# Performance work log

Hardware: AMD Instinct MI355X
Metric: run time of the kernel (lower is better)

## Reference

```python
import jax, jax.numpy as jnp
import numpy as np

ALPHA = 0.2  # LeakyReLU negative slope
NEG_BIG = -9e15


def setup_inputs() -> dict:
    key = jax.random.key(0)
    k1, k2, k3, k4 = jax.random.split(key, 4)
    N, F_IN, F_OUT = 8192, 256, 64
    h = jax.random.normal(k1, (N, F_IN), dtype=jnp.float32)
    # binary dense adjacency (density ~0.5), kept as float32 as in the torch code
    adj = jax.random.randint(k2, (N, N), 0, 2).astype(jnp.float32)
    W = jax.random.normal(k3, (F_IN, F_OUT), dtype=jnp.float32) * 0.05
    a = jax.random.normal(k4, (2 * F_OUT, 1), dtype=jnp.float32) * 0.05
    return {"h": h, "adj": adj, "W": W, "a": a}


def reference(h, adj, W, a):
    F_OUT = W.shape[1]
    Wh = h @ W                               # [N, F]
    # Decomposed concat-attention score: e_ij = LeakyReLU(a1.Wh_i + a2.Wh_j)
    f_src = Wh @ a[:F_OUT, 0]                # [N]
    f_dst = Wh @ a[F_OUT:, 0]                # [N]
    e = f_src[:, None] + f_dst[None, :]      # [N, N]
    e = jnp.where(e > 0, e, ALPHA * e)       # LeakyReLU
    e = jnp.where(adj > 0, e, NEG_BIG)       # mask non-edges
    attention = jax.nn.softmax(e, axis=1)    # row softmax (dropout p=0 -> identity)
    h_prime = attention @ (adj @ Wh)         # note: double propagation as in source
    # concat=True -> ELU
    return jnp.where(h_prime > 0, h_prime, jnp.expm1(h_prime))
```

## Files before the change

### kernel.cpp

```cpp
#include <hip/hip_runtime.h>
#include <hip/hip_bf16.h>


#define N 8192

typedef float f32x4 __attribute__((ext_vector_type(4)));
typedef short s16x8 __attribute__((ext_vector_type(8)));
typedef unsigned long long u64;
typedef u64 u64x2 __attribute__((ext_vector_type(2)));

__device__ __forceinline__ unsigned short f2bf(float x) {
  unsigned u = __float_as_uint(x);
  u += 0x7FFFu + ((u >> 16) & 1u);
  return (unsigned short)(u >> 16);
}
__device__ __forceinline__ unsigned pack2(unsigned short lo, unsigned short hi) {
  return (unsigned)lo | ((unsigned)hi << 16);
}

#define MFMA __builtin_amdgcn_mfma_f32_16x16x32_bf16

__global__ __launch_bounds__(256) void kA(const float* __restrict__ adj,
                                          const float* __restrict__ h,
                                          const float* __restrict__ W,
                                          const float* __restrict__ a,
                                          u64* __restrict__ ML,
                                          unsigned short* __restrict__ Bpack,
                                          float* __restrict__ f,
                                          float* __restrict__ g) {
  const int l = threadIdx.x & 63;
  const int w = threadIdx.x >> 6;
  const int bid = blockIdx.x;
  if ((bid & 1) == 0) {
    const int i = ((bid >> 1) << 2) + w;
    const float* ap = adj + (size_t)i * N + (l << 2);
    u64* mp = ML + (size_t)i * 128;
    f32x4 v0 = *(const f32x4*)(ap);
    f32x4 v1 = *(const f32x4*)(ap + 256);
    f32x4 v2 = *(const f32x4*)(ap + 512);
    f32x4 v3 = *(const f32x4*)(ap + 768);
    for (int cc = 0; cc < 32; cc += 4) {
      const int cn = (cc < 28) ? (cc + 4) : cc;
      f32x4 n0 = *(const f32x4*)(ap + ((cn + 0) << 8));
      f32x4 n1 = *(const f32x4*)(ap + ((cn + 1) << 8));
      f32x4 n2 = *(const f32x4*)(ap + ((cn + 2) << 8));
      f32x4 n3 = *(const f32x4*)(ap + ((cn + 3) << 8));
      u64 b0  = __ballot(v0.x > 0.f), b1  = __ballot(v0.y > 0.f);
      u64 b2  = __ballot(v0.z > 0.f), b3  = __ballot(v0.w > 0.f);
      u64 b4  = __ballot(v1.x > 0.f), b5  = __ballot(v1.y > 0.f);
      u64 b6  = __ballot(v1.z > 0.f), b7  = __ballot(v1.w > 0.f);
      u64 b8  = __ballot(v2.x > 0.f), b9  = __ballot(v2.y > 0.f);
      u64 b10 = __ballot(v2.z > 0.f), b11 = __ballot(v2.w > 0.f);
      u64 b12 = __ballot(v3.x > 0.f), b13 = __ballot(v3.y > 0.f);
      u64 b14 = __ballot(v3.z > 0.f), b15 = __ballot(v3.w > 0.f);
      if (l == 0) {
        u64x2* q = (u64x2*)(mp + (cc << 2));
        u64x2 t0; t0.x = b0;  t0.y = b1;  q[0] = t0;
        u64x2 t1; t1.x = b2;  t1.y = b3;  q[1] = t1;
        u64x2 t2; t2.x = b4;  t2.y = b5;  q[2] = t2;
        u64x2 t3; t3.x = b6;  t3.y = b7;  q[3] = t3;
        u64x2 t4; t4.x = b8;  t4.y = b9;  q[4] = t4;
        u64x2 t5; t5.x = b10; t5.y = b11; q[5] = t5;
        u64x2 t6; t6.x = b12; t6.y = b13; q[6] = t6;
        u64x2 t7; t7.x = b14; t7.y = b15; q[7] = t7;
      }
      v0 = n0; v1 = n1; v2 = n2; v3 = n3;
    }
  } else {
    const int i = ((bid >> 1) << 2) + w;
    const float* hrow = h + (size_t)i * 256;
    float acc = 0.f;
#pragma unroll 4
    for (int kb = 0; kb < 64; ++kb) {
      f32x4 hv = *(const f32x4*)(hrow + (kb << 2));
      acc += hv.x * W[((kb << 2) + 0) * 64 + l];
      acc += hv.y * W[((kb << 2) + 1) * 64 + l];
      acc += hv.z * W[((kb << 2) + 2) * 64 + l];
      acc += hv.w * W[((kb << 2) + 3) * 64 + l];
    }
    float s1 = acc * a[l];
    float s2 = acc * a[64 + l];
#pragma unroll
    for (int d = 32; d > 0; d >>= 1) {
      s1 += __shfl_xor(s1, d);
      s2 += __shfl_xor(s2, d);
    }
    if (l == 0) { f[i] = s1; g[i] = s2; }
    const int kb = i >> 5;
    const int b = l >> 4;
    const int lp = (l & 15) | (((i >> 3) & 3) << 4);
    const int e = i & 7;
    Bpack[(((size_t)(kb * 4 + b)) * 64 + lp) * 8 + e] = f2bf(acc);
  }
}

__global__ __launch_bounds__(512, 4) void k2b(const u64* __restrict__ ML,
                                              const unsigned short* __restrict__ Bpack,
                                              const float* __restrict__ g,
                                              unsigned short* __restrict__ Upack,
                                              float* __restrict__ Gmax) {
  __shared__ float red[8][64][16];
  __shared__ float gred[8][16];
  const int l = threadIdx.x & 63;
  const int w = threadIdx.x >> 6;
  const int i0 = blockIdx.x << 4;
  const int r = l & 15, kg = l >> 4;
  const s16x8* Bv = (const s16x8*)Bpack;
  const u64x2* mrow = (const u64x2*)(ML + (size_t)(i0 + r) * 128);
  const int sh0 = kg << 1;
  f32x4 acc0 = {0.f,0.f,0.f,0.f}, acc1 = acc0, acc2 = acc0, acc3 = acc0;
  float gmx = -INFINITY;
  for (int cc = 0; cc < 4; ++cc) {
    const int c = (w << 2) + cc;
    u64x2 m01 = mrow[(c << 1)], m23 = mrow[(c << 1) + 1];
    const u64 wq0 = m01.x >> sh0, wq1 = m01.y >> sh0,
              wq2 = m23.x >> sh0, wq3 = m23.y >> sh0;
#pragma unroll
    for (int j7 = 0; j7 < 8; ++j7) {
      const int jb = (c << 3) + j7;
      f32x4 g0 = *(const f32x4*)(g + (jb << 5) + (kg << 3));
      f32x4 g1 = *(const f32x4*)(g + (jb << 5) + (kg << 3) + 4);
      const unsigned bit0 = (unsigned)(wq0 >> (j7 << 3)) & 1u;
      const unsigned bit1 = (unsigned)(wq1 >> (j7 << 3)) & 1u;
      const unsigned bit2 = (unsigned)(wq2 >> (j7 << 3)) & 1u;
      const unsigned bit3 = (unsigned)(wq3 >> (j7 << 3)) & 1u;
      const unsigned bit4 = (unsigned)(wq0 >> ((j7 << 3) + 1)) & 1u;
      const unsigned bit5 = (unsigned)(wq1 >> ((j7 << 3) + 1)) & 1u;
      const unsigned bit6 = (unsigned)(wq2 >> ((j7 << 3) + 1)) & 1u;
      const unsigned bit7 = (unsigned)(wq3 >> ((j7 << 3) + 1)) & 1u;
      s16x8 af;
      af[0] = bit0 ? (short)0x3F80 : (short)0;
      af[1] = bit1 ? (short)0x3F80 : (short)0;
      af[2] = bit2 ? (short)0x3F80 : (short)0;
      af[3] = bit3 ? (short)0x3F80 : (short)0;
      af[4] = bit4 ? (short)0x3F80 : (short)0;
      af[5] = bit5 ? (short)0x3F80 : (short)0;
      af[6] = bit6 ? (short)0x3F80 : (short)0;
      af[7] = bit7 ? (short)0x3F80 : (short)0;
      if (bit0) gmx = fmaxf(gmx, g0.x);
      if (bit1) gmx = fmaxf(gmx, g0.y);
      if (bit2) gmx = fmaxf(gmx, g0.z);
      if (bit3) gmx = fmaxf(gmx, g0.w);
      if (bit4) gmx = fmaxf(gmx, g1.x);
      if (bit5) gmx = fmaxf(gmx, g1.y);
      if (bit6) gmx = fmaxf(gmx, g1.z);
      if (bit7) gmx = fmaxf(gmx, g1.w);
      const size_t bi = ((size_t)jb << 8) + l;
      s16x8 f0 = Bv[bi], f1 = Bv[bi + 64], f2 = Bv[bi + 128], f3 = Bv[bi + 192];
      acc0 = MFMA(af, f0, acc0, 0, 0, 0);
      acc1 = MFMA(af, f1, acc1, 0, 0, 0);
      acc2 = MFMA(af, f2, acc2, 0, 0, 0);
      acc3 = MFMA(af, f3, acc3, 0, 0, 0);
    }
  }
  gmx = fmaxf(gmx, __shfl_xor(gmx, 16));
  gmx = fmaxf(gmx, __shfl_xor(gmx, 32));
  if (l < 16) gred[w][l] = gmx;
#pragma unroll
  for (int q = 0; q < 4; ++q) {
    red[w][l][q] = acc0[q]; red[w][l][4 + q] = acc1[q];
    red[w][l][8 + q] = acc2[q]; red[w][l][12 + q] = acc3[q];
  }
  __syncthreads();
  const int tl = threadIdx.x & 63;
  const int b = (threadIdx.x >> 6) & 3;
  const int sE = threadIdx.x >> 8;
  const int reg0 = sE << 1;
  float u0 = 0.f, u1 = 0.f;
#pragma unroll
  for (int w8 = 0; w8 < 8; ++w8) {
    u0 += red[w8][tl][(b << 2) + reg0];
    u1 += red[w8][tl][(b << 2) + reg0 + 1];
  }
  const int k0 = i0 + ((tl >> 4) << 2) + reg0;
  const unsigned pkv = pack2(f2bf(u0), f2bf(u1));
  const int kbD = k0 >> 5, lgrp = (k0 >> 3) & 3, e0 = k0 & 7;
  *(unsigned*)((char*)Upack +
      ((size_t)((kbD << 2) + b) * 64 + ((tl & 15) | (lgrp << 4))) * 16 + (e0 << 1)) = pkv;
  if (threadIdx.x < 16) {
    float gm = gred[0][threadIdx.x];
#pragma unroll
    for (int w8 = 1; w8 < 8; ++w8) gm = fmaxf(gm, gred[w8][threadIdx.x]);
    Gmax[i0 + threadIdx.x] = gm;
  }
}

__global__ __launch_bounds__(512, 4) void k3(const u64* __restrict__ ML,
                                             const unsigned short* __restrict__ Upack,
                                             const float* __restrict__ f,
                                             const float* __restrict__ g,
                                             const float* __restrict__ Gmax,
                                             float* __restrict__ out) {
  __shared__ float red[8][64][16];
  __shared__ float wred[8][16];
  const int l = threadIdx.x & 63;
  const int w = threadIdx.x >> 6;
  const int i0 = blockIdx.x << 4;
  const int r = l & 15, kg = l >> 4;
  const float fi = f[i0 + r];
  float m = fi + Gmax[i0 + r];
  m = fmaxf(m, 0.2f * m);
  const s16x8* Uv = (const s16x8*)Upack;
  const u64x2* mrow = (const u64x2*)(ML + (size_t)(i0 + r) * 128);
  const int sh0 = kg << 1;
  f32x4 acc0 = {0.f,0.f,0.f,0.f}, acc1 = acc0, acc2 = acc0, acc3 = acc0;
  float wsum = 0.f;
  for (int cc = 0; cc < 4; ++cc) {
    const int c = (w << 2) + cc;
    u64x2 m01 = mrow[(c << 1)], m23 = mrow[(c << 1) + 1];
    const u64 wq0 = m01.x >> sh0, wq1 = m01.y >> sh0,
              wq2 = m23.x >> sh0, wq3 = m23.y >> sh0;
#pragma unroll
    for (int j7 = 0; j7 < 8; ++j7) {
      const int jb = (c << 3) + j7;
      f32x4 g0 = *(const f32x4*)(g + (jb << 5) + (kg << 3));
      f32x4 g1 = *(const f32x4*)(g + (jb << 5) + (kg << 3) + 4);
      s16x8 pf;
      float wt;
#define K3W(idx, wq, sh, gv) {                                  \
      const unsigned bit_ = (unsigned)((wq) >> (sh)) & 1u;      \
      float x_ = fi + (gv);                                     \
      float ev_ = fmaxf(x_, 0.2f * x_);                         \
      wt = __expf(ev_ - m);                                     \
      wt = bit_ ? wt : 0.f;                                     \
      wsum += wt; pf[idx] = (short)f2bf(wt); }
      K3W(0, wq0, (j7 << 3),     g0.x)
      K3W(1, wq1, (j7 << 3),     g0.y)
      K3W(2, wq2, (j7 << 3),     g0.z)
      K3W(3, wq3, (j7 << 3),     g0.w)
      K3W(4, wq0, (j7 << 3) + 1, g1.x)
      K3W(5, wq1, (j7 << 3) + 1, g1.y)
      K3W(6, wq2, (j7 << 3) + 1, g1.z)
      K3W(7, wq3, (j7 << 3) + 1, g1.w)
#undef K3W
      const size_t bi = ((size_t)jb << 8) + l;
      s16x8 f0 = Uv[bi], f1 = Uv[bi + 64], f2 = Uv[bi + 128], f3 = Uv[bi + 192];
      acc0 = MFMA(pf, f0, acc0, 0, 0, 0);
      acc1 = MFMA(pf, f1, acc1, 0, 0, 0);
      acc2 = MFMA(pf, f2, acc2, 0, 0, 0);
      acc3 = MFMA(pf, f3, acc3, 0, 0, 0);
    }
  }
  wsum += __shfl_xor(wsum, 16);
  wsum += __shfl_xor(wsum, 32);
  if (l < 16) wred[w][l] = wsum;
#pragma unroll
  for (int q = 0; q < 4; ++q) {
    red[w][l][q] = acc0[q]; red[w][l][4 + q] = acc1[q];
    red[w][l][8 + q] = acc2[q]; red[w][l][12 + q] = acc3[q];
  }
  __syncthreads();
  const int tl = threadIdx.x & 63;
  const int b = (threadIdx.x >> 6) & 3;
  const int sE = threadIdx.x >> 8;
#pragma unroll
  for (int q = 0; q < 2; ++q) {
    const int reg = (sE << 1) + q;
    const int idx = (b << 2) + reg;
    const int row = ((tl >> 4) << 2) + reg;
    float sv = 0.f, dv = 0.f;
#pragma unroll
    for (int w8 = 0; w8 < 8; ++w8) {
      sv += red[w8][tl][idx];
      dv += wred[w8][row];
    }
    dv = (dv > 0.f) ? dv : 1.f;
    float v = sv / dv;
    v = (v > 0.f) ? v : (__expf(v) - 1.f);
    out[(size_t)(i0 + row) * 64 + (b << 4) + (tl & 15)] = v;
  }
}

extern "C" void kernel_launch(void* const* d_in, const int* in_sizes, int n_in,
                              void* d_out, int out_size, void* d_ws, size_t ws_size,
                              hipStream_t stream) {
  const float* h   = (const float*)d_in[0];
  const float* adj = (const float*)d_in[1];
  const float* W   = (const float*)d_in[2];
  const float* a   = (const float*)d_in[3];
  float* out = (float*)d_out;
  char* ws = (char*)d_ws;
  unsigned short* Bpack = (unsigned short*)(ws);
  unsigned short* Upack = (unsigned short*)(ws + (1u << 20));
  float* f    = (float*)(ws + (2u << 20));
  float* g    = (float*)(ws + (2u << 20) + 32768u);
  float* Gmax = (float*)(ws + (2u << 20) + 65536u);
  u64* ML = (u64*)(ws + (3u << 20));

  hipLaunchKernelGGL(kA,  dim3(4096), dim3(256), 0, stream, adj, h, W, a, ML, Bpack, f, g);
  hipLaunchKernelGGL(k2b, dim3(512),  dim3(512), 0, stream, ML, Bpack, g, Upack, Gmax);
  hipLaunchKernelGGL(k3,  dim3(512),  dim3(512), 0, stream, ML, Upack, f, g, Gmax, out);
}
```

Baseline: 140.8 us.

## Factor softmax exponentials into per-row and per-column terms; process 32 rows per block

The per-element exp in the attention kernel is replaced by a product of precomputed per-row factors (exp(f-m), exp(0.2f-m)) and per-column factors (exp(g), exp(0.2g)). The branch of the LeakyReLU is picked by comparing exp(g) against exp(-f). Both the aggregation and attention kernels now handle two 16-row tiles per block, so each B/U fragment load is reused across twice as many MFMAs. This halves the grid to 256 blocks and doubles the accumulator registers and LDS per block. It also drops the occupancy hint, which risks lower occupancy and some numeric drift from the factored exponentials.

```diff
diff --git a/kernel.cpp b/kernel.cpp
--- a/kernel.cpp
+++ b/kernel.cpp
@@ -27,7 +27,9 @@
                                           u64* __restrict__ ML,
                                           unsigned short* __restrict__ Bpack,
                                           float* __restrict__ f,
-                                          float* __restrict__ g) {
+                                          float* __restrict__ g,
+                                          float* __restrict__ expg,
+                                          float* __restrict__ expg2) {
   const int l = threadIdx.x & 63;
   const int w = threadIdx.x >> 6;
   const int bid = blockIdx.x;
@@ -85,7 +87,11 @@
       s1 += __shfl_xor(s1, d);
       s2 += __shfl_xor(s2, d);
     }
-    if (l == 0) { f[i] = s1; g[i] = s2; }
+    if (l == 0) {
+      f[i] = s1; g[i] = s2;
+      expg[i] = __expf(s2);
+      expg2[i] = __expf(0.2f * s2);
+    }
     const int kb = i >> 5;
     const int b = l >> 4;
     const int lp = (l & 15) | (((i >> 3) & 3) << 4);
@@ -94,180 +100,257 @@
   }
 }
 
-__global__ __launch_bounds__(512, 4) void k2b(const u64* __restrict__ ML,
-                                              const unsigned short* __restrict__ Bpack,
-                                              const float* __restrict__ g,
-                                              unsigned short* __restrict__ Upack,
-                                              float* __restrict__ Gmax) {
-  __shared__ float red[8][64][16];
-  __shared__ float gred[8][16];
+__global__ __launch_bounds__(512) void k2b(const u64* __restrict__ ML,
+                                           const unsigned short* __restrict__ Bpack,
+                                           const float* __restrict__ g,
+                                           const float* __restrict__ f,
+                                           unsigned short* __restrict__ Upack,
+                                           float* __restrict__ Av,
+                                           float* __restrict__ Cv) {
+  __shared__ float red[2][8][64][16];
+  __shared__ float gred[2][8][16];
   const int l = threadIdx.x & 63;
   const int w = threadIdx.x >> 6;
-  const int i0 = blockIdx.x << 4;
+  const int i0 = blockIdx.x << 5;
   const int r = l & 15, kg = l >> 4;
   const s16x8* Bv = (const s16x8*)Bpack;
-  const u64x2* mrow = (const u64x2*)(ML + (size_t)(i0 + r) * 128);
+  const u64x2* mrow0 = (const u64x2*)(ML + (size_t)(i0 + r) * 128);
+  const u64x2* mrow1 = (const u64x2*)(ML + (size_t)(i0 + 16 + r) * 128);
   const int sh0 = kg << 1;
-  f32x4 acc0 = {0.f,0.f,0.f,0.f}, acc1 = acc0, acc2 = acc0, acc3 = acc0;
-  float gmx = -INFINITY;
+  f32x4 x0 = {0.f,0.f,0.f,0.f}, x1 = x0, x2 = x0, x3 = x0;
+  f32x4 y0 = x0, y1 = x0, y2 = x0, y3 = x0;
+  float gmx0 = -INFINITY, gmx1 = -INFINITY;
   for (int cc = 0; cc < 4; ++cc) {
     const int c = (w << 2) + cc;
-    u64x2 m01 = mrow[(c << 1)], m23 = mrow[(c << 1) + 1];
-    const u64 wq0 = m01.x >> sh0, wq1 = m01.y >> sh0,
-              wq2 = m23.x >> sh0, wq3 = m23.y >> sh0;
+    u64x2 ma = mrow0[(c << 1)], mb = mrow0[(c << 1) + 1];
+    const u64 xa0 = ma.x >> sh0, xa1 = ma.y >> sh0,
+              xa2 = mb.x >> sh0, xa3 = mb.y >> sh0;
+    u64x2 mc = mrow1[(c << 1)], md = mrow1[(c << 1) + 1];
+    const u64 ya0 = mc.x >> sh0, ya1 = mc.y >> sh0,
+              ya2 = md.x >> sh0, ya3 = md.y >> sh0;
 #pragma unroll
     for (int j7 = 0; j7 < 8; ++j7) {
       const int jb = (c << 3) + j7;
       f32x4 g0 = *(const f32x4*)(g + (jb << 5) + (kg << 3));
       f32x4 g1 = *(const f32x4*)(g + (jb << 5) + (kg << 3) + 4);
-      const unsigned bit0 = (unsigned)(wq0 >> (j7 << 3)) & 1u;
-      const unsigned bit1 = (unsigned)(wq1 >> (j7 << 3)) & 1u;
-      const unsigned bit2 = (unsigned)(wq2 >> (j7 << 3)) & 1u;
-      const unsigned bit3 = (unsigned)(wq3 >> (j7 << 3)) & 1u;
-      const unsigned bit4 = (unsigned)(wq0 >> ((j7 << 3) + 1)) & 1u;
-      const unsigned bit5 = (unsigned)(wq1 >> ((j7 << 3) + 1)) & 1u;
-      const unsigned bit6 = (unsigned)(wq2 >> ((j7 << 3) + 1)) & 1u;
-      const unsigned bit7 = (unsigned)(wq3 >> ((j7 << 3) + 1)) & 1u;
-      s16x8 af;
-      af[0] = bit0 ? (short)0x3F80 : (short)0;
-      af[1] = bit1 ? (short)0x3F80 : (short)0;
-      af[2] = bit2 ? (short)0x3F80 : (short)0;
-      af[3] = bit3 ? (short)0x3F80 : (short)0;
-      af[4] = bit4 ? (short)0x3F80 : (short)0;
-      af[5] = bit5 ? (short)0x3F80 : (short)0;
-      af[6] = bit6 ? (short)0x3F80 : (short)0;
-      af[7] = bit7 ? (short)0x3F80 : (short)0;
-      if (bit0) gmx = fmaxf(gmx, g0.x);
-      if (bit1) gmx = fmaxf(gmx, g0.y);
-      if (bit2) gmx = fmaxf(gmx, g0.z);
-      if (bit3) gmx = fmaxf(gmx, g0.w);
-      if (bit4) gmx = fmaxf(gmx, g1.x);
-      if (bit5) gmx = fmaxf(gmx, g1.y);
-      if (bit6) gmx = fmaxf(gmx, g1.z);
-      if (bit7) gmx = fmaxf(gmx, g1.w);
+      const unsigned p0 = (unsigned)(xa0 >> (j7 << 3)) & 1u;
+      const unsigned p1 = (unsigned)(xa1 >> (j7 << 3)) & 1u;
+      const unsigned p2 = (unsigned)(xa2 >> (j7 << 3)) & 1u;
+      const unsigned p3 = (unsigned)(xa3 >> (j7 << 3)) & 1u;
+      const unsigned p4 = (unsigned)(xa0 >> ((j7 << 3) + 1)) & 1u;
+      const unsigned p5 = (unsigned)(xa1 >> ((j7 << 3) + 1)) & 1u;
+      const unsigned p6 = (unsigned)(xa2 >> ((j7 << 3) + 1)) & 1u;
+      const unsigned p7 = (unsigned)(xa3 >> ((j7 << 3) + 1)) & 1u;
+      const unsigned q0 = (unsigned)(ya0 >> (j7 << 3)) & 1u;
+      const unsigned q1 = (unsigned)(ya1 >> (j7 << 3)) & 1u;
+      const unsigned q2 = (unsigned)(ya2 >> (j7 << 3)) & 1u;
+      const unsigned q3 = (unsigned)(ya3 >> (j7 << 3)) & 1u;
+      const unsigned q4 = (unsigned)(ya0 >> ((j7 << 3) + 1)) & 1u;
+      const unsigned q5 = (unsigned)(ya1 >> ((j7 << 3) + 1)) & 1u;
+      const unsigned q6 = (unsigned)(ya2 >> ((j7 << 3) + 1)) & 1u;
+      const unsigned q7 = (unsigned)(ya3 >> ((j7 << 3) + 1)) & 1u;
+      s16x8 af0, af1;
+      af0[0] = p0 ? (short)0x3F80 : (short)0;
+      af0[1] = p1 ? (short)0x3F80 : (short)0;
+      af0[2] = p2 ? (short)0x3F80 : (short)0;
+      af0[3] = p3 ? (short)0x3F80 : (short)0;
+      af0[4] = p4 ? (short)0x3F80 : (short)0;
+      af0[5] = p5 ? (short)0x3F80 : (short)0;
+      af0[6] = p6 ? (short)0x3F80 : (short)0;
+      af0[7] = p7 ? (short)0x3F80 : (short)0;
+      af1[0] = q0 ? (short)0x3F80 : (short)0;
+      af1[1] = q1 ? (short)0x3F80 : (short)0;
+      af1[2] = q2 ? (short)0x3F80 : (short)0;
+      af1[3] = q3 ? (short)0x3F80 : (short)0;
+      af1[4] = q4 ? (short)0x3F80 : (short)0;
+      af1[5] = q5 ? (short)0x3F80 : (short)0;
+      af1[6] = q6 ? (short)0x3F80 : (short)0;
+      af1[7] = q7 ? (short)0x3F80 : (short)0;
+      if (p0) gmx0 = fmaxf(gmx0, g0.x);
+      if (p1) gmx0 = fmaxf(gmx0, g0.y);
+      if (p2) gmx0 = fmaxf(gmx0, g0.z);
+      if (p3) gmx0 = fmaxf(gmx0, g0.w);
+      if (p4) gmx0 = fmaxf(gmx0, g1.x);
+      if (p5) gmx0 = fmaxf(gmx0, g1.y);
+      if (p6) gmx0 = fmaxf(gmx0, g1.z);
+      if (p7) gmx0 = fmaxf(gmx0, g1.w);
+      if (q0) gmx1 = fmaxf(gmx1, g0.x);
+      if (q1) gmx1 = fmaxf(gmx1, g0.y);
+      if (q2) gmx1 = fmaxf(gmx1, g0.z);
+      if (q3) gmx1 = fmaxf(gmx1, g0.w);
+      if (q4) gmx1 = fmaxf(gmx1, g1.x);
+      if (q5) gmx1 = fmaxf(gmx1, g1.y);
+      if (q6) gmx1 = fmaxf(gmx1, g1.z);
+      if (q7) gmx1 = fmaxf(gmx1, g1.w);
       const size_t bi = ((size_t)jb << 8) + l;
       s16x8 f0 = Bv[bi], f1 = Bv[bi + 64], f2 = Bv[bi + 128], f3 = Bv[bi + 192];
-      acc0 = MFMA(af, f0, acc0, 0, 0, 0);
-      acc1 = MFMA(af, f1, acc1, 0, 0, 0);
-      acc2 = MFMA(af, f2, acc2, 0, 0, 0);
-      acc3 = MFMA(af, f3, acc3, 0, 0, 0);
-    }
-  }
-  gmx = fmaxf(gmx, __shfl_xor(gmx, 16));
-  gmx = fmaxf(gmx, __shfl_xor(gmx, 32));
-  if (l < 16) gred[w][l] = gmx;
+      x0 = MFMA(af0, f0, x0, 0, 0, 0);
+      x1 = MFMA(af0, f1, x1, 0, 0, 0);
+      x2 = MFMA(af0, f2, x2, 0, 0, 0);
+      x3 = MFMA(af0, f3, x3, 0, 0, 0);
+      y0 = MFMA(af1, f0, y0, 0, 0, 0);
+      y1 = MFMA(af1, f1, y1, 0, 0, 0);
+      y2 = MFMA(af1, f2, y2, 0, 0, 0);
+      y3 = MFMA(af1, f3, y3, 0, 0, 0);
+    }
+  }
+  gmx0 = fmaxf(gmx0, __shfl_xor(gmx0, 16));
+  gmx0 = fmaxf(gmx0, __shfl_xor(gmx0, 32));
+  gmx1 = fmaxf(gmx1, __shfl_xor(gmx1, 16));
+  gmx1 = fmaxf(gmx1, __shfl_xor(gmx1, 32));
+  if (l < 16) { gred[0][w][l] = gmx0; gred[1][w][l] = gmx1; }
 #pragma unroll
   for (int q = 0; q < 4; ++q) {
-    red[w][l][q] = acc0[q]; red[w][l][4 + q] = acc1[q];
-    red[w][l][8 + q] = acc2[q]; red[w][l][12 + q] = acc3[q];
+    red[0][w][l][q] = x0[q]; red[0][w][l][4 + q] = x1[q];
+    red[0][w][l][8 + q] = x2[q]; red[0][w][l][12 + q] = x3[q];
+    red[1][w][l][q] = y0[q]; red[1][w][l][4 + q] = y1[q];
+    red[1][w][l][8 + q] = y2[q]; red[1][w][l][12 + q] = y3[q];
   }
   __syncthreads();
   const int tl = threadIdx.x & 63;
   const int b = (threadIdx.x >> 6) & 3;
   const int sE = threadIdx.x >> 8;
   const int reg0 = sE << 1;
-  float u0 = 0.f, u1 = 0.f;
-#pragma unroll
-  for (int w8 = 0; w8 < 8; ++w8) {
-    u0 += red[w8][tl][(b << 2) + reg0];
-    u1 += red[w8][tl][(b << 2) + reg0 + 1];
-  }
-  const int k0 = i0 + ((tl >> 4) << 2) + reg0;
-  const unsigned pkv = pack2(f2bf(u0), f2bf(u1));
-  const int kbD = k0 >> 5, lgrp = (k0 >> 3) & 3, e0 = k0 & 7;
-  *(unsigned*)((char*)Upack +
-      ((size_t)((kbD << 2) + b) * 64 + ((tl & 15) | (lgrp << 4))) * 16 + (e0 << 1)) = pkv;
-  if (threadIdx.x < 16) {
-    float gm = gred[0][threadIdx.x];
-#pragma unroll
-    for (int w8 = 1; w8 < 8; ++w8) gm = fmaxf(gm, gred[w8][threadIdx.x]);
-    Gmax[i0 + threadIdx.x] = gm;
-  }
-}
-
-__global__ __launch_bounds__(512, 4) void k3(const u64* __restrict__ ML,
-                                             const unsigned short* __restrict__ Upack,
-                                             const float* __restrict__ f,
-                                             const float* __restrict__ g,
-                                             const float* __restrict__ Gmax,
-                                             float* __restrict__ out) {
-  __shared__ float red[8][64][16];
-  __shared__ float wred[8][16];
+#pragma unroll
+  for (int s = 0; s < 2; ++s) {
+    float u0 = 0.f, u1 = 0.f;
+#pragma unroll
+    for (int w8 = 0; w8 < 8; ++w8) {
+      u0 += red[s][w8][tl][(b << 2) + reg0];
+      u1 += red[s][w8][tl][(b << 2) + reg0 + 1];
+    }
+    const int k0 = i0 + (s << 4) + ((tl >> 4) << 2) + reg0;
+    const unsigned pkv = pack2(f2bf(u0), f2bf(u1));
+    const int kbD = k0 >> 5, lgrp = (k0 >> 3) & 3, e0 = k0 & 7;
+    *(unsigned*)((char*)Upack +
+        ((size_t)((kbD << 2) + b) * 64 + ((tl & 15) | (lgrp << 4))) * 16 + (e0 << 1)) = pkv;
+  }
+  if (threadIdx.x < 32) {
+    const int s2 = threadIdx.x >> 4, rr = threadIdx.x & 15;
+    float gm = gred[s2][0][rr];
+#pragma unroll
+    for (int w8 = 1; w8 < 8; ++w8) gm = fmaxf(gm, gred[s2][w8][rr]);
+    const int i = i0 + (s2 << 4) + rr;
+    const float fv = f[i];
+    float mm = fv + gm;
+    mm = fmaxf(mm, 0.2f * mm);
+    Av[i] = __expf(fv - mm);
+    Cv[i] = __expf(0.2f * fv - mm);
+  }
+}
+
+__global__ __launch_bounds__(512) void k3(const u64* __restrict__ ML,
+                                          const unsigned short* __restrict__ Upack,
+                                          const float* __restrict__ f,
+                                          const float* __restrict__ expg,
+                                          const float* __restrict__ expg2,
+                                          const float* __restrict__ Av,
+                                          const float* __restrict__ Cv,
+                                          float* __restrict__ out) {
+  __shared__ float red[2][8][64][16];
+  __shared__ float wred[2][8][16];
   const int l = threadIdx.x & 63;
   const int w = threadIdx.x >> 6;
-  const int i0 = blockIdx.x << 4;
+  const int i0 = blockIdx.x << 5;
   const int r = l & 15, kg = l >> 4;
-  const float fi = f[i0 + r];
-  float m = fi + Gmax[i0 + r];
-  m = fmaxf(m, 0.2f * m);
+  const float enf0 = __expf(-f[i0 + r]);
+  const float enf1 = __expf(-f[i0 + 16 + r]);
+  const float Ar0 = Av[i0 + r],      Cr0 = Cv[i0 + r];
+  const float Ar1 = Av[i0 + 16 + r], Cr1 = Cv[i0 + 16 + r];
   const s16x8* Uv = (const s16x8*)Upack;
-  const u64x2* mrow = (const u64x2*)(ML + (size_t)(i0 + r) * 128);
+  const u64x2* mrow0 = (const u64x2*)(ML + (size_t)(i0 + r) * 128);
+  const u64x2* mrow1 = (const u64x2*)(ML + (size_t)(i0 + 16 + r) * 128);
   const int sh0 = kg << 1;
-  f32x4 acc0 = {0.f,0.f,0.f,0.f}, acc1 = acc0, acc2 = acc0, acc3 = acc0;
-  float wsum = 0.f;
+  f32x4 x0 = {0.f,0.f,0.f,0.f}, x1 = x0, x2 = x0, x3 = x0;
+  f32x4 y0 = x0, y1 = x0, y2 = x0, y3 = x0;
+  float ws0 = 0.f, ws1 = 0.f;
   for (int cc = 0; cc < 4; ++cc) {
     const int c = (w << 2) + cc;
-    u64x2 m01 = mrow[(c << 1)], m23 = mrow[(c << 1) + 1];
-    const u64 wq0 = m01.x >> sh0, wq1 = m01.y >> sh0,
-              wq2 = m23.x >> sh0, wq3 = m23.y >> sh0;
+    u64x2 ma = mrow0[(c << 1)], mb = mrow0[(c << 1) + 1];
+    const u64 xa0 = ma.x >> sh0, xa1 = ma.y >> sh0,
+              xa2 = mb.x >> sh0, xa3 = mb.y >> sh0;
+    u64x2 mc = mrow1[(c << 1)], md = mrow1[(c << 1) + 1];
+    const u64 ya0 = mc.x >> sh0, ya1 = mc.y >> sh0,
+              ya2 = md.x >> sh0, ya3 = md.y >> sh0;
 #pragma unroll
     for (int j7 = 0; j7 < 8; ++j7) {
       const int jb = (c << 3) + j7;
-      f32x4 g0 = *(const f32x4*)(g + (jb << 5) + (kg << 3));
-      f32x4 g1 = *(const f32x4*)(g + (jb << 5) + (kg << 3) + 4);
-      s16x8 pf;
-      float wt;
-#define K3W(idx, wq, sh, gv) {                                  \
-      const unsigned bit_ = (unsigned)((wq) >> (sh)) & 1u;      \
-      float x_ = fi + (gv);                                     \
-      float ev_ = fmaxf(x_, 0.2f * x_);                         \
-      wt = __expf(ev_ - m);                                     \
-      wt = bit_ ? wt : 0.f;                                     \
-      wsum += wt; pf[idx] = (short)f2bf(wt); }
-      K3W(0, wq0, (j7 << 3),     g0.x)
-      K3W(1, wq1, (j7 << 3),     g0.y)
-      K3W(2, wq2, (j7 << 3),     g0.z)
-      K3W(3, wq3, (j7 << 3),     g0.w)
-      K3W(4, wq0, (j7 << 3) + 1, g1.x)
-      K3W(5, wq1, (j7 << 3) + 1, g1.y)
-      K3W(6, wq2, (j7 << 3) + 1, g1.z)
-      K3W(7, wq3, (j7 << 3) + 1, g1.w)
+      f32x4 eg0 = *(const f32x4*)(expg + (jb << 5) + (kg << 3));
+      f32x4 eg1 = *(const f32x4*)(expg + (jb << 5) + (kg << 3) + 4);
+      f32x4 eh0 = *(const f32x4*)(expg2 + (jb << 5) + (kg << 3));
+      f32x4 eh1 = *(const f32x4*)(expg2 + (jb << 5) + (kg << 3) + 4);
+      s16x8 pf0, pf1;
+#define K3W(pf, idx, wq, sh, egv, ehv, enf, Ar, Cr, wsv) {   \
+      const unsigned bit_ = (unsigned)((wq) >> (sh)) & 1u;   \
+      const bool sg_ = (egv) > (enf);                        \
+      float t_ = sg_ ? (Ar) : (Cr);                          \
+      float u_ = sg_ ? (egv) : (ehv);                        \
+      float wt_ = t_ * u_;                                   \
+      wt_ = bit_ ? wt_ : 0.f;                                \
+      wsv += wt_; pf[idx] = (short)f2bf(wt_); }
+      K3W(pf0, 0, xa0, (j7 << 3),     eg0.x, eh0.x, enf0, Ar0, Cr0, ws0)
+      K3W(pf0, 1, xa1, (j7 << 3),     eg0.y, eh0.y, enf0, Ar0, Cr0, ws0)
+      K3W(pf0, 2, xa2, (j7 << 3),     eg0.z, eh0.z, enf0, Ar0, Cr0, ws0)
+      K3W(pf0, 3, xa3, (j7 << 3),     eg0.w, eh0.w, enf0, Ar0, Cr0, ws0)
+      K3W(pf0, 4, xa0, (j7 << 3) + 1, eg1.x, eh1.x, enf0, Ar0, Cr0, ws0)
+      K3W(pf0, 5, xa1, (j7 << 3) + 1, eg1.y, eh1.y, enf0, Ar0, Cr0, ws0)
+      K3W(pf0, 6, xa2, (j7 << 3) + 1, eg1.z, eh1.z, enf0, Ar0, Cr0, ws0)
+      K3W(pf0, 7, xa3, (j7 << 3) + 1, eg1.w, eh1.w, enf0, Ar0, Cr0, ws0)
+      K3W(pf1, 0, ya0, (j7 << 3),     eg0.x, eh0.x, enf1, Ar1, Cr1, ws1)
+      K3W(pf1, 1, ya1, (j7 << 3),     eg0.y, eh0.y, enf1, Ar1, Cr1, ws1)
+      K3W(pf1, 2, ya2, (j7 << 3),     eg0.z, eh0.z, enf1, Ar1, Cr1, ws1)
+      K3W(pf1, 3, ya3, (j7 << 3),     eg0.w, eh0.w, enf1, Ar1, Cr1, ws1)
+      K3W(pf1, 4, ya0, (j7 << 3) + 1, eg1.x, eh1.x, enf1, Ar1, Cr1, ws1)
+      K3W(pf1, 5, ya1, (j7 << 3) + 1, eg1.y, eh1.y, enf1, Ar1, Cr1, ws1)
+      K3W(pf1, 6, ya2, (j7 << 3) + 1, eg1.z, eh1.z, enf1, Ar1, Cr1, ws1)
+      K3W(pf1, 7, ya3, (j7 << 3) + 1, eg1.w, eh1.w, enf1, Ar1, Cr1, ws1)
 #undef K3W
       const size_t bi = ((size_t)jb << 8) + l;
       s16x8 f0 = Uv[bi], f1 = Uv[bi + 64], f2 = Uv[bi + 128], f3 = Uv[bi + 192];
-      acc0 = MFMA(pf, f0, acc0, 0, 0, 0);
-      acc1 = MFMA(pf, f1, acc1, 0, 0, 0);
-      acc2 = MFMA(pf, f2, acc2, 0, 0, 0);
-      acc3 = MFMA(pf, f3, acc3, 0, 0, 0);
-    }
-  }
-  wsum += __shfl_xor(wsum, 16);
-  wsum += __shfl_xor(wsum, 32);
-  if (l < 16) wred[w][l] = wsum;
+      x0 = MFMA(pf0, f0, x0, 0, 0, 0);
+      x1 = MFMA(pf0, f1, x1, 0, 0, 0);
+      x2 = MFMA(pf0, f2, x2, 0, 0, 0);
+      x3 = MFMA(pf0, f3, x3, 0, 0, 0);
+      y0 = MFMA(pf1, f0, y0, 0, 0, 0);
+      y1 = MFMA(pf1, f1, y1, 0, 0, 0);
+      y2 = MFMA(pf1, f2, y2, 0, 0, 0);
+      y3 = MFMA(pf1, f3, y3, 0, 0, 0);
+    }
+  }
+  ws0 += __shfl_xor(ws0, 16);
+  ws0 += __shfl_xor(ws0, 32);
+  ws1 += __shfl_xor(ws1, 16);
+  ws1 += __shfl_xor(ws1, 32);
+  if (l < 16) { wred[0][w][l] = ws0; wred[1][w][l] = ws1; }
 #pragma unroll
   for (int q = 0; q < 4; ++q) {
-    red[w][l][q] = acc0[q]; red[w][l][4 + q] = acc1[q];
-    red[w][l][8 + q] = acc2[q]; red[w][l][12 + q] = acc3[q];
+    red[0][w][l][q] = x0[q]; red[0][w][l][4 + q] = x1[q];
+    red[0][w][l][8 + q] = x2[q]; red[0][w][l][12 + q] = x3[q];
+    red[1][w][l][q] = y0[q]; red[1][w][l][4 + q] = y1[q];
+    red[1][w][l][8 + q] = y2[q]; red[1][w][l][12 + q] = y3[q];
   }
   __syncthreads();
   const int tl = threadIdx.x & 63;
   const int b = (threadIdx.x >> 6) & 3;
   const int sE = threadIdx.x >> 8;
 #pragma unroll
-  for (int q = 0; q < 2; ++q) {
-    const int reg = (sE << 1) + q;
-    const int idx = (b << 2) + reg;
-    const int row = ((tl >> 4) << 2) + reg;
-    float sv = 0.f, dv = 0.f;
-#pragma unroll
-    for (int w8 = 0; w8 < 8; ++w8) {
-      sv += red[w8][tl][idx];
-      dv += wred[w8][row];
-    }
-    dv = (dv > 0.f) ? dv : 1.f;
-    float v = sv / dv;
-    v = (v > 0.f) ? v : (__expf(v) - 1.f);
-    out[(size_t)(i0 + row) * 64 + (b << 4) + (tl & 15)] = v;
+  for (int s = 0; s < 2; ++s) {
+#pragma unroll
+    for (int q = 0; q < 2; ++q) {
+      const int reg = (sE << 1) + q;
+      const int idx = (b << 2) + reg;
+      const int row = ((tl >> 4) << 2) + reg;
+      float sv = 0.f, dv = 0.f;
+#pragma unroll
+      for (int w8 = 0; w8 < 8; ++w8) {
+        sv += red[s][w8][tl][idx];
+        dv += wred[s][w8][row];
+      }
+      dv = (dv > 0.f) ? dv : 1.f;
+      float v = sv / dv;
+      v = (v > 0.f) ? v : (__expf(v) - 1.f);
+      out[(size_t)(i0 + (s << 4) + row) * 64 + (b << 4) + (tl & 15)] = v;
+    }
   }
 }
 
@@ -282,12 +365,18 @@
   char* ws = (char*)d_ws;
   unsigned short* Bpack = (unsigned short*)(ws);
   unsigned short* Upack = (unsigned short*)(ws + (1u << 20));
-  float* f    = (float*)(ws + (2u << 20));
-  float* g    = (float*)(ws + (2u << 20) + 32768u);
-  float* Gmax = (float*)(ws + (2u << 20) + 65536u);
+  float* f     = (float*)(ws + (2u << 20));
+  float* g     = (float*)(ws + (2u << 20) + 1u * 32768u);
+  float* expg  = (float*)(ws + (2u << 20) + 2u * 32768u);
+  float* expg2 = (float*)(ws + (2u << 20) + 3u * 32768u);
+  float* Av    = (float*)(ws + (2u << 20) + 4u * 32768u);
+  float* Cv    = (float*)(ws + (2u << 20) + 5u * 32768u);
   u64* ML = (u64*)(ws + (3u << 20));
 
-  hipLaunchKernelGGL(kA,  dim3(4096), dim3(256), 0, stream, adj, h, W, a, ML, Bpack, f, g);
-  hipLaunchKernelGGL(k2b, dim3(512),  dim3(512), 0, stream, ML, Bpack, g, Upack, Gmax);
-  hipLaunchKernelGGL(k3,  dim3(512),  dim3(512), 0, stream, ML, Upack, f, g, Gmax, out);
-}
+  hipLaunchKernelGGL(kA,  dim3(4096), dim3(256), 0, stream,
+                     adj, h, W, a, ML, Bpack, f, g, expg, expg2);
+  hipLaunchKernelGGL(k2b, dim3(256), dim3(512), 0, stream,
+                     ML, Bpack, g, f, Upack, Av, Cv);
+  hipLaunchKernelGGL(k3,  dim3(256), dim3(512), 0, stream,
+                     ML, Upack, f, expg, expg2, Av, Cv, out);
+}
```

Result: no change. 138.3 us (-1.8%).
